# Kernel tuning notes

Hardware: AMD Instinct MI355X
Metric: run time of the kernel (lower is better)

## Reference

```python
import jax, jax.numpy as jnp
import numpy as np

# DRAW-SN dims (enc_size must equal dec_size: mu/sigma Linears declared on dec_size are applied to h_enc)
T, A, B, N = 16, 128, 128, 32
Z, DEC, ENC = 512, 2048, 2048
BATCH = 512
IN_ENC = 2 * N * N + DEC
LOG2PI = float(np.log(2.0 * np.pi))


def setup_inputs() -> dict:
    key = jax.random.key(0)
    k = jax.random.split(key, 14)
    s = 0.02
    return {
        "x": jax.random.uniform(k[0], (BATCH, A * B), dtype=jnp.float32),
        "eps": jax.random.normal(k[1], (T, BATCH, Z), dtype=jnp.float32),
        # PyTorch LSTMCell weights, gate order (i,f,g,o); b = b_ih + b_hh merged
        "enc_Wih": jax.random.normal(k[2], (4 * ENC, IN_ENC), dtype=jnp.float32) * s,
        "enc_Whh": jax.random.normal(k[3], (4 * ENC, ENC), dtype=jnp.float32) * s,
        "enc_b": jax.random.normal(k[4], (4 * ENC,), dtype=jnp.float32) * s,
        "dec_Wih": jax.random.normal(k[5], (4 * DEC, Z), dtype=jnp.float32) * s,
        "dec_Whh": jax.random.normal(k[6], (4 * DEC, DEC), dtype=jnp.float32) * s,
        "dec_b": jax.random.normal(k[7], (4 * DEC,), dtype=jnp.float32) * s,
        "mu_W": jax.random.normal(k[8], (Z, ENC), dtype=jnp.float32) * s,
        "mu_b": jnp.zeros((Z,), jnp.float32),
        "sig_W": jax.random.normal(k[9], (Z, ENC), dtype=jnp.float32) * s,
        "sig_b": jnp.zeros((Z,), jnp.float32),
        "attn_W": jax.random.normal(k[10], (5, DEC), dtype=jnp.float32) * s,
        "attn_b": jnp.zeros((5,), jnp.float32),
        "w_W": jax.random.normal(k[11], (N * N, DEC), dtype=jnp.float32) * s,
        "w_b": jnp.zeros((N * N,), jnp.float32),
    }


def _lstm(xin, h, c, Wih, Whh, b):
    g = xin @ Wih.T + h @ Whh.T + b
    i, f, gg, o = jnp.split(g, 4, axis=1)
    c_new = jax.nn.sigmoid(f) * c + jax.nn.sigmoid(i) * jnp.tanh(gg)
    h_new = jax.nn.sigmoid(o) * jnp.tanh(c_new)
    return h_new, c_new


def _attn(h_dec, attn_W, attn_b):
    p = h_dec @ attn_W.T + attn_b  # (batch, 5)
    gx = (A + 1) / 2 * (p[:, 0] + 1)
    gy = (B + 1) / 2 * (p[:, 1] + 1)
    sigma2 = jnp.exp(p[:, 2])
    delta = (max(A, B) - 1) / (N - 1) * jnp.exp(p[:, 3])
    gamma = jnp.exp(p[:, 4])
    rng = jnp.arange(N, dtype=p.dtype) - N / 2 - 0.5
    mu_x = gx[:, None] + rng * delta[:, None]  # (batch, N)
    mu_y = gy[:, None] + rng * delta[:, None]

    def fmat(size, mu):
        grid = jnp.arange(size, dtype=p.dtype)
        t = (grid[None, None, :] - mu[:, :, None]) / (2 * sigma2[:, None, None])
        F = jnp.exp(-t * t)  # (batch, N, size)
        return F / (jnp.sum(F, axis=2, keepdims=True) + 1e-9)

    return fmat(A, mu_x), fmat(B, mu_y), gamma


def _glimpse(img, Fx, Fy, bsz):
    # Fy (b,N,B) @ img (b,B,A) @ Fx^T (b,A,N) -> (b,N,N)
    return jnp.einsum('bnB,bBa,bma->bnm', Fy, img.reshape(bsz, B, A), Fx).reshape(bsz, N * N)


def _mdl(h):
    # getHistoryStats (history=None -> stats of h itself, COMP=0) + getMDL with RN=True, s=ones
    mean = jnp.mean(h)
    std = jnp.std(h, ddof=1)
    log_p = -0.5 * ((h - mean) / std) ** 2 - jnp.log(std) - 0.5 * LOG2PI
    lse = jax.nn.logsumexp(log_p)
    # both branches of the COMP update equal log(exp(COMP) + sum exp(log_p)) with COMP=0
    COMP = jnp.logaddexp(jnp.float32(0.0), lse)
    l = COMP - lse  # log(s)=0 for s=ones
    return l * h


def reference(x, eps, enc_Wih, enc_Whh, enc_b, dec_Wih, dec_Whh, dec_b,
              mu_W, mu_b, sig_W, sig_b, attn_W, attn_b, w_W, w_b):
    bsz = x.shape[0]

    def step(carry, e):
        h_enc, c_enc, h_dec, c_dec, canvas = carry
        x_hat = x - jax.nn.sigmoid(canvas)
        # read
        Fx, Fy, gamma = _attn(h_dec, attn_W, attn_b)
        r = jnp.concatenate([_glimpse(x, Fx, Fy, bsz) * gamma[:, None],
                             _glimpse(x_hat, Fx, Fy, bsz) * gamma[:, None]], axis=1)
        # encoder + MDL renorm
        h_enc, c_enc = _lstm(jnp.concatenate([r, h_dec], axis=1), h_enc, c_enc,
                             enc_Wih, enc_Whh, enc_b)
        h_enc = _mdl(h_enc)
        # sampleQ
        mu = h_enc @ mu_W.T + mu_b
        sigma = jnp.exp(h_enc @ sig_W.T + sig_b)
        z = mu + sigma * e
        # decoder + MDL renorm
        h_dec_new, c_dec = _lstm(z, h_dec, c_dec, dec_Wih, dec_Whh, dec_b)
        h_dec_new = _mdl(h_dec_new)
        # write: Fy^T @ w @ Fx -> (b,B,A), divided by gamma
        Fx2, Fy2, gamma2 = _attn(h_dec_new, attn_W, attn_b)
        w = (h_dec_new @ w_W.T + w_b).reshape(bsz, N, N)
        wr = jnp.einsum('bnB,bnm,bma->bBa', Fy2, w, Fx2).reshape(bsz, A * B)
        canvas = canvas + wr / gamma2[:, None]
        return (h_enc, c_enc, h_dec_new, c_dec, canvas), None

    init = (jnp.zeros((bsz, ENC), x.dtype), jnp.zeros((bsz, ENC), x.dtype),
            jnp.zeros((bsz, DEC), x.dtype), jnp.zeros((bsz, DEC), x.dtype),
            jnp.zeros((bsz, A * B), x.dtype))
    carry, _ = jax.lax.scan(step, init, eps)
    return carry[4]  # final canvas cs[T-1], shape (batch, A*B)
```

## Files before the change

kernel.cpp:

```cpp
#include <hip/hip_runtime.h>
#include <math.h>

#define BSZ   512
#define TSTEPS 16
#define HID   2048
#define G4    8192
#define ZD    512
#define ABF   16384
#define LOG2PI_F 1.8378770664093453f

typedef float  f32x4  __attribute__((ext_vector_type(4)));
typedef __bf16 bf16x8 __attribute__((ext_vector_type(8)));
typedef unsigned short u16;
typedef u16 u16x4 __attribute__((ext_vector_type(4)));
typedef u16 u16x8v __attribute__((ext_vector_type(8)));
union bfcast { u16x8v u; bf16x8 b; };

__device__ __forceinline__ u16 f2bf(float f){
  union { float f; unsigned u; } v; v.f = f;
  unsigned u = v.u;
  return (u16)((u + 0x7FFFu + ((u >> 16) & 1u)) >> 16);
}
__device__ __forceinline__ float bf2f(u16 u){
  union { unsigned u; float f; } v; v.u = ((unsigned)u) << 16; return v.f;
}
__device__ __forceinline__ float sigm(float x){ return 1.f/(1.f + expf(-x)); }

__device__ __forceinline__ void load_lds16(const void* g, void* l){
  __builtin_amdgcn_global_load_lds(
      (const __attribute__((address_space(1))) void*)g,
      (__attribute__((address_space(3))) void*)l, 16, 0, 0);
}

__device__ __forceinline__ float wsum(float v){
  #pragma unroll
  for (int o = 32; o; o >>= 1) v += __shfl_down(v, o, 64);
  return v;
}

__global__ __launch_bounds__(256) void zero_kernel(float* __restrict__ p, int n4){
  int i = blockIdx.x*256 + threadIdx.x;
  const int st = gridDim.x*256;
  f32x4 z = {0.f,0.f,0.f,0.f};
  for (; i < n4; i += st) ((f32x4*)p)[i] = z;
}

__global__ __launch_bounds__(256) void cvt_kernel(const float* __restrict__ s, u16* __restrict__ d, int n4){
  int i = blockIdx.x*256 + threadIdx.x;
  const int st = gridDim.x*256;
  for (; i < n4; i += st){
    f32x4 v = ((const f32x4*)s)[i];
    u16x4 o;
    o[0]=f2bf(v[0]); o[1]=f2bf(v[1]); o[2]=f2bf(v[2]); o[3]=f2bf(v[3]);
    ((u16x4*)d)[i] = o;
  }
}

__global__ __launch_bounds__(256) void read_fused(
    const u16* __restrict__ x_bf, const float* __restrict__ canvas,
    const u16* __restrict__ h_dec_bf, const float* __restrict__ attnW,
    const float* __restrict__ attn_b, u16* __restrict__ r_bf)
{
  const int b = blockIdx.x;
  const int tid = threadIdx.x;
  const int wave = tid >> 6;
  const int lane = tid & 63;
  const int lr = lane & 15;
  const int lq = lane >> 4;
  __shared__ float red[4][5];
  __shared__ float prm[5];
  __shared__ float rowsum[32][9];
  __shared__ __align__(16) u16 Fxb[32*128];
  __shared__ __align__(16) u16 Fyb[32*128];
  __shared__ __align__(16) u16 Ttx[32*136];
  __shared__ __align__(16) u16 Ttxh[32*136];

  {
    float a0=0,a1=0,a2=0,a3=0,a4=0;
    const u16* h = h_dec_bf + (size_t)b*HID;
    for (int k = tid; k < HID; k += 256){
      const float hv = bf2f(h[k]);
      a0 += hv*attnW[k];
      a1 += hv*attnW[HID + k];
      a2 += hv*attnW[2*HID + k];
      a3 += hv*attnW[3*HID + k];
      a4 += hv*attnW[4*HID + k];
    }
    a0 = wsum(a0); a1 = wsum(a1); a2 = wsum(a2); a3 = wsum(a3); a4 = wsum(a4);
    if (lane == 0){
      red[wave][0]=a0; red[wave][1]=a1; red[wave][2]=a2; red[wave][3]=a3; red[wave][4]=a4;
    }
  }
  __syncthreads();
  if (tid < 5){
    const float p = red[0][tid]+red[1][tid]+red[2][tid]+red[3][tid] + attn_b[tid];
    float v;
    if (tid <= 1)      v = 64.5f*(p + 1.f);
    else if (tid == 2) v = 1.f/(2.f*expf(p));
    else if (tid == 3) v = (127.f/31.f)*expf(p);
    else               v = expf(p);
    prm[tid] = v;
  }
  __syncthreads();
  const float gx = prm[0], gy = prm[1], i2s = prm[2], dl = prm[3], gm = prm[4];

  auto genF = [&](float g0, u16* dst){
    const int rr = tid >> 3;
    const int asub = tid & 7;
    const float mu = g0 + ((float)rr - 16.5f)*dl;
    float s = 0.f;
    for (int a = asub*16; a < asub*16 + 16; a++){
      const float t = ((float)a - mu)*i2s;
      s += expf(-t*t);
    }
    rowsum[rr][asub] = s;
    __syncthreads();
    if (tid < 32){
      float tot = 0.f;
      #pragma unroll
      for (int j = 0; j < 8; j++) tot += rowsum[tid][j];
      rowsum[tid][8] = 1.f/(tot + 1e-9f);
    }
    __syncthreads();
    for (int i = tid; i < 4096; i += 256){
      const int n = i >> 7, a = i & 127;
      const float mu2 = g0 + ((float)n - 16.5f)*dl;
      const float t = ((float)a - mu2)*i2s;
      const float v = expf(-t*t)*rowsum[n][8];
      const int pos = (a >> 3) ^ (n & 7);
      dst[n*128 + pos*8 + (a & 7)] = f2bf(v);
    }
    __syncthreads();
  };
  genF(gx, Fxb);
  genF(gy, Fyb);

  const u16*   xb = x_bf   + (size_t)b*ABF;
  const float* cb = canvas + (size_t)b*ABF;
  f32x4 Cx[2][2], Ch[2][2];
  #pragma unroll
  for (int i = 0; i < 2; i++)
    #pragma unroll
    for (int j = 0; j < 2; j++){ Cx[i][j] = (f32x4){0,0,0,0}; Ch[i][j] = (f32x4){0,0,0,0}; }

  #pragma unroll
  for (int mt = 0; mt < 2; mt++){
    const int row = wave*32 + mt*16 + lr;
    bfcast ax[4], ah[4];
    #pragma unroll
    for (int ks = 0; ks < 4; ks++){
      const int base = row*128 + ks*32 + lq*8;
      ax[ks].u = *(const u16x8v*)&xb[base];
      f32x4 c0 = *(const f32x4*)&cb[base];
      f32x4 c1 = *(const f32x4*)&cb[base + 4];
      #pragma unroll
      for (int j = 0; j < 4; j++){
        ah[ks].u[j]   = f2bf(bf2f(ax[ks].u[j])   - sigm(c0[j]));
        ah[ks].u[4+j] = f2bf(bf2f(ax[ks].u[4+j]) - sigm(c1[j]));
      }
    }
    #pragma unroll
    for (int nt = 0; nt < 2; nt++){
      #pragma unroll
      for (int ks = 0; ks < 4; ks++){
        const int pos = (ks*4 + lq) ^ (lr & 7);
        bf16x8 bf_ = *(const bf16x8*)&Fxb[(nt*16 + lr)*128 + pos*8];
        Cx[mt][nt] = __builtin_amdgcn_mfma_f32_16x16x32_bf16(ax[ks].b, bf_, Cx[mt][nt], 0, 0, 0);
        Ch[mt][nt] = __builtin_amdgcn_mfma_f32_16x16x32_bf16(ah[ks].b, bf_, Ch[mt][nt], 0, 0, 0);
      }
    }
  }
  #pragma unroll
  for (int mt = 0; mt < 2; mt++)
    #pragma unroll
    for (int nt = 0; nt < 2; nt++)
      #pragma unroll
      for (int r = 0; r < 4; r++){
        const int m  = nt*16 + lr;
        const int B_ = wave*32 + mt*16 + lq*4 + r;
        Ttx[m*136 + B_]  = f2bf(Cx[mt][nt][r]);
        Ttxh[m*136 + B_] = f2bf(Ch[mt][nt][r]);
      }
  __syncthreads();

  const int mat = wave >> 1;
  const u16* Tt = mat ? Ttxh : Ttx;
  const int ntl = wave & 1;
  f32x4 R[2];
  R[0] = (f32x4){0,0,0,0}; R[1] = (f32x4){0,0,0,0};
  #pragma unroll
  for (int ks = 0; ks < 4; ks++){
    const int pos = (ks*4 + lq) ^ (lr & 7);
    bf16x8 af = *(const bf16x8*)&Fyb[(ntl*16 + lr)*128 + pos*8];
    #pragma unroll
    for (int mt = 0; mt < 2; mt++){
      bf16x8 bf_ = *(const bf16x8*)&Tt[(mt*16 + lr)*136 + ks*32 + lq*8];
      R[mt] = __builtin_amdgcn_mfma_f32_16x16x32_bf16(af, bf_, R[mt], 0, 0, 0);
    }
  }
  #pragma unroll
  for (int mt = 0; mt < 2; mt++){
    const int m = mt*16 + lr;
    #pragma unroll
    for (int r = 0; r < 4; r++){
      const int n = ntl*16 + lq*4 + r;
      r_bf[(size_t)b*2048 + mat*1024 + n*32 + m] = f2bf(R[mt][r]*gm);
    }
  }
}

struct Slice { const u16* A; const u16* W; const u16* Whi; float* C; int lda, ldw, K, pad; };
struct Slices { Slice s[4]; };

template<int BM, int BN>
__global__ __launch_bounds__(256) void gemm_bt(Slices sl, int nsplit, int ldc)
{
  constexpr int BK = 64;
  constexpr int FI = BM/32;
  constexpr int FJ = BN/32;
  __shared__ __align__(16) u16 Asm[BM*BK];
  __shared__ __align__(16) u16 Bsm[BN*BK];
  const int tid  = threadIdx.x;
  const int wave = tid >> 6;
  const int lane = tid & 63;
  const int wm = wave & 1, wn = wave >> 1;
  const int m0 = blockIdx.y * BM;
  const int n0 = blockIdx.x * BN;
  const Slice& sp = sl.s[blockIdx.z];
  const u16* Ap = sp.A;
  const u16* Wp = sp.W;
  const int lda = sp.lda, ldw = sp.ldw, K = sp.K;
  if (nsplit > 0 && n0 >= nsplit) Wp = sp.Whi - (size_t)nsplit * ldw;
  float* C = sp.C;

  f32x4 acc[FI][FJ];
  #pragma unroll
  for (int i = 0; i < FI; i++)
    #pragma unroll
    for (int j = 0; j < FJ; j++) acc[i][j] = (f32x4){0.f,0.f,0.f,0.f};

  const int lr = lane & 15;
  const int lq = lane >> 4;

  for (int kt = 0; kt < K; kt += BK){
    __syncthreads();
    constexpr int NCA = BM*BK/8;
    #pragma unroll
    for (int it = 0; it < NCA/256; it++){
      const int cb = it*256 + wave*64;
      const int c  = cb + lane;
      const int row = c >> 3;
      const int c8  = (c & 7) ^ (row & 7);
      load_lds16(Ap + (size_t)(m0 + row)*lda + kt + c8*8, &Asm[cb*8]);
    }
    constexpr int NCB = BN*BK/8;
    #pragma unroll
    for (int it = 0; it < NCB/256; it++){
      const int cb = it*256 + wave*64;
      const int c  = cb + lane;
      const int row = c >> 3;
      const int c8  = (c & 7) ^ (row & 7);
      load_lds16(Wp + (size_t)(n0 + row)*ldw + kt + c8*8, &Bsm[cb*8]);
    }
    __syncthreads();
    #pragma unroll
    for (int ks = 0; ks < 2; ks++){
      bf16x8 af[FI], bfr[FJ];
      #pragma unroll
      for (int i = 0; i < FI; i++){
        const int row = wm*(BM/2) + i*16 + lr;
        const int xx = (ks*4 + lq) ^ (row & 7);
        af[i] = *(const bf16x8*)&Asm[row*BK + xx*8];
      }
      #pragma unroll
      for (int j = 0; j < FJ; j++){
        const int row = wn*(BN/2) + j*16 + lr;
        const int xx = (ks*4 + lq) ^ (row & 7);
        bfr[j] = *(const bf16x8*)&Bsm[row*BK + xx*8];
      }
      #pragma unroll
      for (int i = 0; i < FI; i++)
        #pragma unroll
        for (int j = 0; j < FJ; j++)
          acc[i][j] = __builtin_amdgcn_mfma_f32_16x16x32_bf16(af[i], bfr[j], acc[i][j], 0, 0, 0);
    }
  }
  #pragma unroll
  for (int i = 0; i < FI; i++){
    const int gm = m0 + wm*(BM/2) + i*16 + lq*4;
    #pragma unroll
    for (int j = 0; j < FJ; j++){
      const int gn = n0 + wn*(BN/2) + j*16 + lr;
      #pragma unroll
      for (int r = 0; r < 4; r++)
        C[(size_t)(gm + r)*ldc + gn] = acc[i][j][r];
    }
  }
}

__global__ __launch_bounds__(256) void lstm_kernel(
    const float* __restrict__ g, const float* __restrict__ bias,
    float* __restrict__ c, float* __restrict__ h, float* __restrict__ ps)
{
  const int idx = blockIdx.x*256 + threadIdx.x;
  const int m = idx >> 9;
  const int q = idx & 511;
  const size_t gb = (size_t)m*G4 + q*4;
  const float* g1 = g + 4194304;
  const float* g2 = g + 2*4194304;
  f32x4 gi = *(const f32x4*)&g[gb]         + *(const f32x4*)&g1[gb]         + *(const f32x4*)&g2[gb]         + *(const f32x4*)&bias[q*4];
  f32x4 gf = *(const f32x4*)&g[gb+HID]     + *(const f32x4*)&g1[gb+HID]     + *(const f32x4*)&g2[gb+HID]     + *(const f32x4*)&bias[HID+q*4];
  f32x4 gg = *(const f32x4*)&g[gb+2*HID]   + *(const f32x4*)&g1[gb+2*HID]   + *(const f32x4*)&g2[gb+2*HID]   + *(const f32x4*)&bias[2*HID+q*4];
  f32x4 go = *(const f32x4*)&g[gb+3*HID]   + *(const f32x4*)&g1[gb+3*HID]   + *(const f32x4*)&g2[gb+3*HID]   + *(const f32x4*)&bias[3*HID+q*4];
  const size_t cb = (size_t)m*HID + q*4;
  f32x4 cv = *(const f32x4*)&c[cb];
  f32x4 cn, hn;
  #pragma unroll
  for (int k = 0; k < 4; k++){
    const float ck = sigm(gf[k])*cv[k] + sigm(gi[k])*tanhf(gg[k]);
    cn[k] = ck;
    hn[k] = sigm(go[k])*tanhf(ck);
  }
  *(f32x4*)&c[cb] = cn;
  *(f32x4*)&h[cb] = hn;
  float s1 = hn[0]+hn[1]+hn[2]+hn[3];
  float s2 = hn[0]*hn[0]+hn[1]*hn[1]+hn[2]*hn[2]+hn[3]*hn[3];
  s1 = wsum(s1); s2 = wsum(s2);
  __shared__ float r1[4], r2[4];
  const int w = threadIdx.x >> 6;
  if ((threadIdx.x & 63) == 0){ r1[w] = s1; r2[w] = s2; }
  __syncthreads();
  if (threadIdx.x == 0){
    ps[blockIdx.x]        = r1[0]+r1[1]+r1[2]+r1[3];
    ps[1024 + blockIdx.x] = r2[0]+r2[1]+r2[2]+r2[3];
  }
}

__global__ __launch_bounds__(256) void sumexp_kernel(
    const float* __restrict__ h, const float* __restrict__ ps, float* __restrict__ pe)
{
  const int tid = threadIdx.x;
  float t1 = 0.f, t2 = 0.f;
  for (int i = tid; i < 1024; i += 256){ t1 += ps[i]; t2 += ps[1024 + i]; }
  t1 = wsum(t1); t2 = wsum(t2);
  __shared__ float r1[4], r2[4];
  const int w = tid >> 6;
  if ((tid & 63) == 0){ r1[w] = t1; r2[w] = t2; }
  __syncthreads();
  __shared__ float mh[2];
  if (tid == 0){
    const float S1 = r1[0]+r1[1]+r1[2]+r1[3];
    const float S2 = r2[0]+r2[1]+r2[2]+r2[3];
    const float mean = S1*(1.f/1048576.f);
    const float var  = (S2 - 1048576.f*mean*mean)*(1.f/1048575.f);
    mh[0] = mean; mh[1] = 1.f/sqrtf(var);
  }
  __syncthreads();
  const float mean = mh[0], istd = mh[1];
  float se = 0.f;
  for (int i = blockIdx.x*256 + tid; i < (1<<18); i += 256*256){
    f32x4 v = ((const f32x4*)h)[i];
    #pragma unroll
    for (int k = 0; k < 4; k++){
      const float u = (v[k] - mean)*istd;
      se += expf(-0.5f*u*u);
    }
  }
  se = wsum(se);
  __shared__ float r3[4];
  if ((tid & 63) == 0) r3[w] = se;
  __syncthreads();
  if (tid == 0) pe[blockIdx.x] = r3[0]+r3[1]+r3[2]+r3[3];
}

__global__ __launch_bounds__(256) void scale_kernel(
    const float* __restrict__ h, const float* __restrict__ ps,
    const float* __restrict__ pe, u16* __restrict__ hb)
{
  const int tid = threadIdx.x;
  float t1 = 0.f, t2 = 0.f;
  for (int i = tid; i < 1024; i += 256){ t1 += ps[i]; t2 += ps[1024 + i]; }
  float t3 = pe[tid];
  t1 = wsum(t1); t2 = wsum(t2); t3 = wsum(t3);
  __shared__ float r1[4], r2[4], r3[4];
  const int w = tid >> 6;
  if ((tid & 63) == 0){ r1[w] = t1; r2[w] = t2; r3[w] = t3; }
  __syncthreads();
  __shared__ float lsh;
  if (tid == 0){
    const float S1 = r1[0]+r1[1]+r1[2]+r1[3];
    const float S2 = r2[0]+r2[1]+r2[2]+r2[3];
    const float SE = r3[0]+r3[1]+r3[2]+r3[3];
    const float mean = S1*(1.f/1048576.f);
    const float var  = (S2 - 1048576.f*mean*mean)*(1.f/1048575.f);
    const float stdv = sqrtf(var);
    const float lse = logf(SE) - logf(stdv) - 0.5f*LOG2PI_F;
    lsh = fmaxf(-lse, 0.f) + log1pf(expf(-fabsf(lse)));
  }
  __syncthreads();
  const float l = lsh;
  const int i = blockIdx.x*256 + tid;
  f32x4 v = ((const f32x4*)h)[i];
  u16x4 o;
  #pragma unroll
  for (int k = 0; k < 4; k++) o[k] = f2bf(v[k]*l);
  ((u16x4*)hb)[i] = o;
}

__global__ __launch_bounds__(256) void z_kernel(
    const float* __restrict__ zp, const float* __restrict__ mu_b,
    const float* __restrict__ sig_b, const float* __restrict__ ep, u16* __restrict__ zo)
{
  const int idx = blockIdx.x*256 + threadIdx.x;
  const int m = idx >> 7;
  const int q = idx & 127;
  const size_t base = (size_t)m*1024 + q*4;
  f32x4 mu = *(const f32x4*)&zp[base] + *(const f32x4*)&zp[524288 + base]
           + *(const f32x4*)&zp[2*524288 + base] + *(const f32x4*)&zp[3*524288 + base]
           + *(const f32x4*)&mu_b[q*4];
  f32x4 ls = *(const f32x4*)&zp[base+512] + *(const f32x4*)&zp[524288 + base+512]
           + *(const f32x4*)&zp[2*524288 + base+512] + *(const f32x4*)&zp[3*524288 + base+512]
           + *(const f32x4*)&sig_b[q*4];
  f32x4 ev = *(const f32x4*)&ep[(size_t)m*512 + q*4];
  u16x4 o;
  #pragma unroll
  for (int k = 0; k < 4; k++) o[k] = f2bf(mu[k] + expf(ls[k])*ev[k]);
  ((u16x4*)zo)[idx] = o;
}

__global__ __launch_bounds__(256) void write_fused(
    const float* __restrict__ wp, const float* __restrict__ w_b,
    const u16* __restrict__ h_dec_bf, const float* __restrict__ attnW,
    const float* __restrict__ attn_b, float* __restrict__ canvas)
{
  const int b = blockIdx.x;
  const int tid = threadIdx.x;
  __shared__ float red[4][5];
  __shared__ float prm[5];
  __shared__ float inv[32];
  __shared__ float sW[1024];
  __shared__ __align__(16) float sF[32*132];
  __shared__ float sU[128*33];

  {
    float a0=0,a1=0,a2=0,a3=0,a4=0;
    const u16* h = h_dec_bf + (size_t)b*HID;
    for (int k = tid; k < HID; k += 256){
      const float hv = bf2f(h[k]);
      a0 += hv*attnW[k];
      a1 += hv*attnW[HID + k];
      a2 += hv*attnW[2*HID + k];
      a3 += hv*attnW[3*HID + k];
      a4 += hv*attnW[4*HID + k];
    }
    a0 = wsum(a0); a1 = wsum(a1); a2 = wsum(a2); a3 = wsum(a3); a4 = wsum(a4);
    if ((tid & 63) == 0){
      const int w = tid >> 6;
      red[w][0]=a0; red[w][1]=a1; red[w][2]=a2; red[w][3]=a3; red[w][4]=a4;
    }
  }
  for (int i = tid; i < 1024; i += 256)
    sW[i] = wp[(size_t)b*1024 + i] + wp[524288 + (size_t)b*1024 + i]
          + wp[2*524288 + (size_t)b*1024 + i] + wp[3*524288 + (size_t)b*1024 + i] + w_b[i];
  __syncthreads();
  if (tid < 5){
    const float p = red[0][tid]+red[1][tid]+red[2][tid]+red[3][tid] + attn_b[tid];
    float v;
    if (tid <= 1)      v = 64.5f*(p + 1.f);
    else if (tid == 2) v = 1.f/(2.f*expf(p));
    else if (tid == 3) v = (127.f/31.f)*expf(p);
    else               v = expf(p);
    prm[tid] = v;
  }
  __syncthreads();
  const float gx = prm[0], gy = prm[1], i2s = prm[2], dl = prm[3], gm = prm[4];

  auto genF = [&](float g0){
    for (int i = tid; i < 4096; i += 256){
      const int n = i >> 7, a = i & 127;
      const float mu = g0 + ((float)n - 16.5f)*dl;
      const float t = ((float)a - mu)*i2s;
      sF[n*132 + a] = expf(-t*t);
    }
    __syncthreads();
    if (tid < 32){
      float ssum = 0.f;
      for (int a = 0; a < 128; a++) ssum += sF[tid*132 + a];
      inv[tid] = 1.f/(ssum + 1e-9f);
    }
    __syncthreads();
    for (int i = tid; i < 4096; i += 256)
      sF[(i >> 7)*132 + (i & 127)] *= inv[i >> 7];
    __syncthreads();
  };

  genF(gy);
  {
    const int Bg = tid & 31, mg = tid >> 5;
    float acc[4][4] = {};
    for (int n = 0; n < 32; n++){
      float fy[4], wv[4];
      #pragma unroll
      for (int i = 0; i < 4; i++) fy[i] = sF[n*132 + Bg + 32*i];
      #pragma unroll
      for (int j = 0; j < 4; j++) wv[j] = sW[n*32 + mg*4 + j];
      #pragma unroll
      for (int i = 0; i < 4; i++)
        #pragma unroll
        for (int j = 0; j < 4; j++) acc[i][j] += fy[i]*wv[j];
    }
    #pragma unroll
    for (int i = 0; i < 4; i++)
      #pragma unroll
      for (int j = 0; j < 4; j++)
        sU[(Bg + 32*i)*33 + mg*4 + j] = acc[i][j];
  }
  __syncthreads();
  genF(gx);
  {
    const int Bg = tid & 31, ag = tid >> 5;
    float acc[64];
    #pragma unroll
    for (int k = 0; k < 64; k++) acc[k] = 0.f;
    for (int mm = 0; mm < 32; mm++){
      float u[4];
      #pragma unroll
      for (int i = 0; i < 4; i++) u[i] = sU[(Bg + 32*i)*33 + mm];
      f32x4 fx[4];
      #pragma unroll
      for (int k = 0; k < 4; k++) fx[k] = *(const f32x4*)&sF[mm*132 + ag*16 + k*4];
      #pragma unroll
      for (int i = 0; i < 4; i++)
        #pragma unroll
        for (int k = 0; k < 4; k++)
          #pragma unroll
          for (int cc = 0; cc < 4; cc++)
            acc[i*16 + k*4 + cc] += u[i]*fx[k][cc];
    }
    const float ig = 1.f/gm;
    #pragma unroll
    for (int i = 0; i < 4; i++){
      const int B_ = Bg + 32*i;
      #pragma unroll
      for (int k = 0; k < 4; k++){
        float* cp = &canvas[(size_t)b*ABF + B_*128 + ag*16 + k*4];
        f32x4 cv = *(const f32x4*)cp;
        #pragma unroll
        for (int cc = 0; cc < 4; cc++) cv[cc] += acc[i*16 + k*4 + cc]*ig;
        *(f32x4*)cp = cv;
      }
    }
  }
}

extern "C" void kernel_launch(void* const* d_in, const int* in_sizes, int n_in,
                              void* d_out, int out_size, void* d_ws, size_t ws_size,
                              hipStream_t stream)
{
  (void)in_sizes; (void)n_in; (void)out_size; (void)ws_size;
  const float* x      = (const float*)d_in[0];
  const float* eps    = (const float*)d_in[1];
  const float* encWih = (const float*)d_in[2];
  const float* encWhh = (const float*)d_in[3];
  const float* enc_b  = (const float*)d_in[4];
  const float* decWih = (const float*)d_in[5];
  const float* decWhh = (const float*)d_in[6];
  const float* dec_b  = (const float*)d_in[7];
  const float* muW    = (const float*)d_in[8];
  const float* mu_b   = (const float*)d_in[9];
  const float* sigW   = (const float*)d_in[10];
  const float* sig_b  = (const float*)d_in[11];
  const float* attnW  = (const float*)d_in[12];
  const float* attn_b = (const float*)d_in[13];
  const float* wW     = (const float*)d_in[14];
  const float* w_b    = (const float*)d_in[15];
  float* canvas = (float*)d_out;

  char* wsb = (char*)d_ws;
  size_t off = 0;
  auto alloc = [&](size_t bytes)->char*{
    char* p = wsb + off; off += (bytes + 255) & ~(size_t)255; return p;
  };
  float* c_enc    = (float*)alloc(1048576*4);
  float* c_dec    = (float*)alloc(1048576*4);
  u16*   h_enc_bf = (u16*)  alloc(1048576*2);
  u16*   h_dec_bf = (u16*)  alloc(1048576*2);
  const size_t state_bytes = off;
  float* ps    = (float*)alloc(2304*4);
  float* pe    = (float*)alloc(256*4);
  float* h_tmp = (float*)alloc(1048576*4);
  float* g_buf = (float*)alloc((size_t)3*4194304*4);
  u16*   r_bf  = (u16*)  alloc(1048576*2);
  u16*   z_bf  = (u16*)  alloc(262144*2);
  float* zbuf  = (float*)alloc((size_t)4*524288*4);
  float* wbuf  = (float*)alloc((size_t)4*524288*4);
  u16*   x_bf  = (u16*)  alloc((size_t)8388608*2);
  u16* wih_bf  = (u16*)alloc((size_t)33554432*2);
  u16* whh_bf  = (u16*)alloc((size_t)16777216*2);
  u16* dwih_bf = (u16*)alloc((size_t)4194304*2);
  u16* dwhh_bf = (u16*)alloc((size_t)16777216*2);
  u16* muw_bf  = (u16*)alloc((size_t)1048576*2);
  u16* sigw_bf = (u16*)alloc((size_t)1048576*2);
  u16* ww_bf   = (u16*)alloc((size_t)2097152*2);

  zero_kernel<<<1024, 256, 0, stream>>>((float*)wsb, (int)(state_bytes/16));
  zero_kernel<<<2048, 256, 0, stream>>>(canvas, (ABF/4)*BSZ);
  cvt_kernel<<<2048, 256, 0, stream>>>(x,      x_bf,    8388608/4);
  cvt_kernel<<<2048, 256, 0, stream>>>(encWih, wih_bf,  33554432/4);
  cvt_kernel<<<2048, 256, 0, stream>>>(encWhh, whh_bf,  16777216/4);
  cvt_kernel<<<1024, 256, 0, stream>>>(decWih, dwih_bf, 4194304/4);
  cvt_kernel<<<2048, 256, 0, stream>>>(decWhh, dwhh_bf, 16777216/4);
  cvt_kernel<<<512,  256, 0, stream>>>(muW,    muw_bf,  1048576/4);
  cvt_kernel<<<512,  256, 0, stream>>>(sigW,   sigw_bf, 1048576/4);
  cvt_kernel<<<512,  256, 0, stream>>>(wW,     ww_bf,   2097152/4);

  float* g0 = g_buf;
  float* g1 = g_buf + 4194304;
  float* g2 = g_buf + 2*4194304;

  Slices enc_sl = {};
  enc_sl.s[0] = { r_bf,            wih_bf,          nullptr, g0, HID, 2*HID, HID, 0 };
  enc_sl.s[1] = { h_dec_bf,        wih_bf + HID,    nullptr, g1, HID, 2*HID, HID, 0 };
  enc_sl.s[2] = { h_enc_bf,        whh_bf,          nullptr, g2, HID, HID,   HID, 0 };

  Slices dec_sl = {};
  dec_sl.s[0] = { z_bf,            dwih_bf,         nullptr, g0, ZD,  ZD,    ZD,   0 };
  dec_sl.s[1] = { h_dec_bf,        dwhh_bf,         nullptr, g1, HID, HID,   1024, 0 };
  dec_sl.s[2] = { h_dec_bf + 1024, dwhh_bf + 1024,  nullptr, g2, HID, HID,   1024, 0 };

  Slices ms_sl = {}, w_sl = {};
  for (int k = 0; k < 4; k++){
    ms_sl.s[k] = { h_enc_bf + 512*k, muw_bf + 512*k, sigw_bf + 512*k, zbuf + (size_t)k*524288, HID, HID, 512, 0 };
    w_sl.s[k]  = { h_dec_bf + 512*k, ww_bf  + 512*k, nullptr,         wbuf + (size_t)k*524288, HID, HID, 512, 0 };
  }

  for (int t = 0; t < TSTEPS; t++){
    read_fused<<<512, 256, 0, stream>>>(x_bf, canvas, h_dec_bf, attnW, attn_b, r_bf);
    gemm_bt<64,128><<<dim3(64,8,3), 256, 0, stream>>>(enc_sl, 0, G4);
    lstm_kernel<<<1024, 256, 0, stream>>>(g_buf, enc_b, c_enc, h_tmp, ps);
    sumexp_kernel<<<256, 256, 0, stream>>>(h_tmp, ps, pe);
    scale_kernel<<<1024, 256, 0, stream>>>(h_tmp, ps, pe, h_enc_bf);
    gemm_bt<64,64><<<dim3(16,8,4), 256, 0, stream>>>(ms_sl, 512, 1024);
    z_kernel<<<256, 256, 0, stream>>>(zbuf, mu_b, sig_b, eps + (size_t)t*BSZ*ZD, z_bf);
    gemm_bt<64,128><<<dim3(64,8,3), 256, 0, stream>>>(dec_sl, 0, G4);
    lstm_kernel<<<1024, 256, 0, stream>>>(g_buf, dec_b, c_dec, h_tmp, ps);
    sumexp_kernel<<<256, 256, 0, stream>>>(h_tmp, ps, pe);
    scale_kernel<<<1024, 256, 0, stream>>>(h_tmp, ps, pe, h_dec_bf);
    gemm_bt<64,64><<<dim3(16,8,4), 256, 0, stream>>>(w_sl, 0, 1024);
    write_fused<<<512, 256, 0, stream>>>(wbuf, w_b, h_dec_bf, attnW, attn_b, canvas);
  }
}
```

Measured before the change: 4.342 ms.

## Concatenate LSTM inputs and weights, use 256x256 double-buffered split-K GEMM

Packs the encoder input [r, h_dec, h_enc] and decoder input [z, h_dec] into single concatenated activation buffers, with matching concatenated bf16 weight matrices. The LSTM gate GEMMs then run as one uniform 4-way split-K problem on a new 256x256-tile, 512-thread, LDS double-buffered MFMA kernel. The LSTM kernel sums four partial buffers instead of three. This aims to raise arithmetic intensity and balance work across slices. The cost is an extra partial-sum read and write, plus a scale kernel that writes h_dec to two places.

After: 4.137 ms. -4.7%, faster.

```diff
diff --git a/kernel.cpp b/kernel.cpp
--- a/kernel.cpp
+++ b/kernel.cpp
@@ -7,6 +7,8 @@
 #define G4    8192
 #define ZD    512
 #define ABF   16384
+#define ENCK  6144
+#define DECK  2560
 #define LOG2PI_F 1.8378770664093453f
 
 typedef float  f32x4  __attribute__((ext_vector_type(4)));
@@ -56,10 +58,26 @@
   }
 }
 
+__global__ __launch_bounds__(256) void cvt_strided_kernel(
+    const float* __restrict__ s, u16* __restrict__ d,
+    int n4, int sh, int cmask, int dstride, int coloff)
+{
+  int i = blockIdx.x*256 + threadIdx.x;
+  const int st = gridDim.x*256;
+  for (; i < n4; i += st){
+    f32x4 v = ((const f32x4*)s)[i];
+    u16x4 o;
+    o[0]=f2bf(v[0]); o[1]=f2bf(v[1]); o[2]=f2bf(v[2]); o[3]=f2bf(v[3]);
+    const int row = i >> sh;
+    const int c4  = i & cmask;
+    *(u16x4*)&d[(size_t)row*dstride + coloff + c4*4] = o;
+  }
+}
+
 __global__ __launch_bounds__(256) void read_fused(
     const u16* __restrict__ x_bf, const float* __restrict__ canvas,
-    const u16* __restrict__ h_dec_bf, const float* __restrict__ attnW,
-    const float* __restrict__ attn_b, u16* __restrict__ r_bf)
+    const u16* __restrict__ hd, const float* __restrict__ attnW,
+    const float* __restrict__ attn_b, u16* __restrict__ r_out)
 {
   const int b = blockIdx.x;
   const int tid = threadIdx.x;
@@ -77,7 +95,7 @@
 
   {
     float a0=0,a1=0,a2=0,a3=0,a4=0;
-    const u16* h = h_dec_bf + (size_t)b*HID;
+    const u16* h = hd + (size_t)b*DECK;
     for (int k = tid; k < HID; k += 256){
       const float hv = bf2f(h[k]);
       a0 += hv*attnW[k];
@@ -204,7 +222,7 @@
     #pragma unroll
     for (int r = 0; r < 4; r++){
       const int n = ntl*16 + lq*4 + r;
-      r_bf[(size_t)b*2048 + mat*1024 + n*32 + m] = f2bf(R[mt][r]*gm);
+      r_out[(size_t)b*ENCK + mat*1024 + n*32 + m] = f2bf(R[mt][r]*gm);
     }
   }
 }
@@ -298,6 +316,109 @@
   }
 }
 
+__global__ __launch_bounds__(512, 2) void gemm256(Slices sl, int ldc)
+{
+  __shared__ __align__(16) u16 Asm[2][256*64];
+  __shared__ __align__(16) u16 Bsm[2][256*64];
+  const int tid  = threadIdx.x;
+  const int wave = tid >> 6;
+  const int lane = tid & 63;
+  const int lr = lane & 15;
+  const int lq = lane >> 4;
+  const int wm = wave >> 2;
+  const int wn = wave & 3;
+
+  const int bid = blockIdx.x;
+  const int wg  = (bid & 7)*32 + (bid >> 3);
+  const int bx  = wg & 31;
+  const int by  = (wg >> 5) & 1;
+  const int bz  = wg >> 6;
+  const int m0 = by*256, n0 = bx*256;
+  const Slice& sp = sl.s[bz];
+  const u16* __restrict__ Ap = sp.A;
+  const u16* __restrict__ Wp = sp.W;
+  float* __restrict__ C = sp.C;
+  const int lda = sp.lda, ldw = sp.ldw;
+  const int nt = sp.K >> 6;
+
+  f32x4 acc[8][4];
+  #pragma unroll
+  for (int i = 0; i < 8; i++)
+    #pragma unroll
+    for (int j = 0; j < 4; j++) acc[i][j] = (f32x4){0.f,0.f,0.f,0.f};
+
+  auto stage = [&](int kt, int bsel){
+    const int kcol = kt << 6;
+    #pragma unroll
+    for (int it = 0; it < 4; it++){
+      const int cbk = it*512 + wave*64;
+      const int c   = cbk + lane;
+      const int row = c >> 3;
+      const int c8  = (c & 7) ^ (row & 7);
+      load_lds16(Ap + (size_t)(m0 + row)*lda + kcol + c8*8, &Asm[bsel][cbk*8]);
+    }
+    #pragma unroll
+    for (int it = 0; it < 4; it++){
+      const int cbk = it*512 + wave*64;
+      const int c   = cbk + lane;
+      const int row = c >> 3;
+      const int c8  = (c & 7) ^ (row & 7);
+      load_lds16(Wp + (size_t)(n0 + row)*ldw + kcol + c8*8, &Bsm[bsel][cbk*8]);
+    }
+  };
+
+  stage(0, 0);
+  for (int t = 0; t < nt; t++){
+    const int cur = t & 1;
+    if (t + 1 < nt){
+      stage(t + 1, cur ^ 1);
+      __builtin_amdgcn_sched_barrier(0);
+      asm volatile("s_waitcnt vmcnt(8)" ::: "memory");
+    } else {
+      asm volatile("s_waitcnt vmcnt(0)" ::: "memory");
+    }
+    __builtin_amdgcn_s_barrier();
+    __builtin_amdgcn_sched_barrier(0);
+
+    bf16x8 bfr[2][4];
+    #pragma unroll
+    for (int ks = 0; ks < 2; ks++)
+      #pragma unroll
+      for (int j = 0; j < 4; j++){
+        const int row = wn*64 + j*16 + lr;
+        const int xx = (ks*4 + lq) ^ (row & 7);
+        bfr[ks][j] = *(const bf16x8*)&Bsm[cur][row*64 + xx*8];
+      }
+    #pragma unroll
+    for (int i = 0; i < 8; i++){
+      const int row = wm*128 + i*16 + lr;
+      const bf16x8 a0 = *(const bf16x8*)&Asm[cur][row*64 + ((lq    ) ^ (row & 7))*8];
+      const bf16x8 a1 = *(const bf16x8*)&Asm[cur][row*64 + ((4 + lq) ^ (row & 7))*8];
+      __builtin_amdgcn_s_setprio(1);
+      #pragma unroll
+      for (int j = 0; j < 4; j++){
+        acc[i][j] = __builtin_amdgcn_mfma_f32_16x16x32_bf16(a0, bfr[0][j], acc[i][j], 0, 0, 0);
+        acc[i][j] = __builtin_amdgcn_mfma_f32_16x16x32_bf16(a1, bfr[1][j], acc[i][j], 0, 0, 0);
+      }
+      __builtin_amdgcn_s_setprio(0);
+    }
+    __builtin_amdgcn_sched_barrier(0);
+    __builtin_amdgcn_s_barrier();
+  }
+
+  #pragma unroll
+  for (int i = 0; i < 8; i++){
+    const int gmr = m0 + wm*128 + i*16 + lq*4;
+    #pragma unroll
+    for (int j = 0; j < 4; j++){
+      const int gn = n0 + wn*64 + j*16 + lr;
+      #pragma unroll
+      for (int r = 0; r < 4; r++)
+        C[(size_t)(gmr + r)*ldc + gn] = acc[i][j][r];
+    }
+  }
+}
+
 __global__ __launch_bounds__(256) void lstm_kernel(
     const float* __restrict__ g, const float* __restrict__ bias,
     float* __restrict__ c, float* __restrict__ h, float* __restrict__ ps)
@@ -308,10 +429,11 @@
   const size_t gb = (size_t)m*G4 + q*4;
   const float* g1 = g + 4194304;
   const float* g2 = g + 2*4194304;
-  f32x4 gi = *(const f32x4*)&g[gb]         + *(const f32x4*)&g1[gb]         + *(const f32x4*)&g2[gb]         + *(const f32x4*)&bias[q*4];
-  f32x4 gf = *(const f32x4*)&g[gb+HID]     + *(const f32x4*)&g1[gb+HID]     + *(const f32x4*)&g2[gb+HID]     + *(const f32x4*)&bias[HID+q*4];
-  f32x4 gg = *(const f32x4*)&g[gb+2*HID]   + *(const f32x4*)&g1[gb+2*HID]   + *(const f32x4*)&g2[gb+2*HID]   + *(const f32x4*)&bias[2*HID+q*4];
-  f32x4 go = *(const f32x4*)&g[gb+3*HID]   + *(const f32x4*)&g1[gb+3*HID]   + *(const f32x4*)&g2[gb+3*HID]   + *(const f32x4*)&bias[3*HID+q*4];
+  const float* g3 = g + 3*4194304;
+  f32x4 gi = *(const f32x4*)&g[gb]         + *(const f32x4*)&g1[gb]         + *(const f32x4*)&g2[gb]         + *(const f32x4*)&g3[gb]         + *(const f32x4*)&bias[q*4];
+  f32x4 gf = *(const f32x4*)&g[gb+HID]     + *(const f32x4*)&g1[gb+HID]     + *(const f32x4*)&g2[gb+HID]     + *(const f32x4*)&g3[gb+HID]     + *(const f32x4*)&bias[HID+q*4];
+  f32x4 gg = *(const f32x4*)&g[gb+2*HID]   + *(const f32x4*)&g1[gb+2*HID]   + *(const f32x4*)&g2[gb+2*HID]   + *(const f32x4*)&g3[gb+2*HID]   + *(const f32x4*)&bias[2*HID+q*4];
+  f32x4 go = *(const f32x4*)&g[gb+3*HID]   + *(const f32x4*)&g1[gb+3*HID]   + *(const f32x4*)&g2[gb+3*HID]   + *(const f32x4*)&g3[gb+3*HID]   + *(const f32x4*)&bias[3*HID+q*4];
   const size_t cb = (size_t)m*HID + q*4;
   f32x4 cv = *(const f32x4*)&c[cb];
   f32x4 cn, hn;
@@ -375,7 +497,8 @@
 
 __global__ __launch_bounds__(256) void scale_kernel(
     const float* __restrict__ h, const float* __restrict__ ps,
-    const float* __restrict__ pe, u16* __restrict__ hb)
+    const float* __restrict__ pe, u16* __restrict__ d1, int ld1,
+    u16* __restrict__ d2, int ld2)
 {
   const int tid = threadIdx.x;
   float t1 = 0.f, t2 = 0.f;
@@ -400,11 +523,14 @@
   __syncthreads();
   const float l = lsh;
   const int i = blockIdx.x*256 + tid;
+  const int row = i >> 9;
+  const int c4  = i & 511;
   f32x4 v = ((const f32x4*)h)[i];
   u16x4 o;
   #pragma unroll
   for (int k = 0; k < 4; k++) o[k] = f2bf(v[k]*l);
-  ((u16x4*)hb)[i] = o;
+  *(u16x4*)&d1[(size_t)row*ld1 + c4*4] = o;
+  if (d2) *(u16x4*)&d2[(size_t)row*ld2 + c4*4] = o;
 }
 
 __global__ __launch_bounds__(256) void z_kernel(
@@ -425,12 +551,12 @@
   u16x4 o;
   #pragma unroll
   for (int k = 0; k < 4; k++) o[k] = f2bf(mu[k] + expf(ls[k])*ev[k]);
-  ((u16x4*)zo)[idx] = o;
+  *(u16x4*)&zo[(size_t)m*DECK + q*4] = o;
 }
 
 __global__ __launch_bounds__(256) void write_fused(
     const float* __restrict__ wp, const float* __restrict__ w_b,
-    const u16* __restrict__ h_dec_bf, const float* __restrict__ attnW,
+    const u16* __restrict__ hd, const float* __restrict__ attnW,
     const float* __restrict__ attn_b, float* __restrict__ canvas)
 {
   const int b = blockIdx.x;
@@ -444,7 +570,7 @@
 
   {
     float a0=0,a1=0,a2=0,a3=0,a4=0;
-    const u16* h = h_dec_bf + (size_t)b*HID;
+    const u16* h = hd + (size_t)b*DECK;
     for (int k = tid; k < HID; k += 256){
       const float hv = bf2f(h[k]);
       a0 += hv*attnW[k];
@@ -581,72 +707,62 @@
   auto alloc = [&](size_t bytes)->char*{
     char* p = wsb + off; off += (bytes + 255) & ~(size_t)255; return p;
   };
-  float* c_enc    = (float*)alloc(1048576*4);
-  float* c_dec    = (float*)alloc(1048576*4);
-  u16*   h_enc_bf = (u16*)  alloc(1048576*2);
-  u16*   h_dec_bf = (u16*)  alloc(1048576*2);
+  float* c_enc = (float*)alloc(1048576*4);
+  float* c_dec = (float*)alloc(1048576*4);
+  u16*   encA  = (u16*)  alloc((size_t)BSZ*ENCK*2);
+  u16*   decA  = (u16*)  alloc((size_t)BSZ*DECK*2);
   const size_t state_bytes = off;
   float* ps    = (float*)alloc(2304*4);
   float* pe    = (float*)alloc(256*4);
   float* h_tmp = (float*)alloc(1048576*4);
-  float* g_buf = (float*)alloc((size_t)3*4194304*4);
-  u16*   r_bf  = (u16*)  alloc(1048576*2);
-  u16*   z_bf  = (u16*)  alloc(262144*2);
-  float* zbuf  = (float*)alloc((size_t)4*524288*4);
-  float* wbuf  = (float*)alloc((size_t)4*524288*4);
+  float* g_buf = (float*)alloc((size_t)4*4194304*4);
+  float* zbuf  = g_buf;
+  float* wbuf  = g_buf + 2097152;
   u16*   x_bf  = (u16*)  alloc((size_t)8388608*2);
-  u16* wih_bf  = (u16*)alloc((size_t)33554432*2);
-  u16* whh_bf  = (u16*)alloc((size_t)16777216*2);
-  u16* dwih_bf = (u16*)alloc((size_t)4194304*2);
-  u16* dwhh_bf = (u16*)alloc((size_t)16777216*2);
+  u16* encW    = (u16*)alloc((size_t)G4*ENCK*2);
+  u16* decW    = (u16*)alloc((size_t)G4*DECK*2);
   u16* muw_bf  = (u16*)alloc((size_t)1048576*2);
   u16* sigw_bf = (u16*)alloc((size_t)1048576*2);
   u16* ww_bf   = (u16*)alloc((size_t)2097152*2);
 
   zero_kernel<<<1024, 256, 0, stream>>>((float*)wsb, (int)(state_bytes/16));
   zero_kernel<<<2048, 256, 0, stream>>>(canvas, (ABF/4)*BSZ);
-  cvt_kernel<<<2048, 256, 0, stream>>>(x,      x_bf,    8388608/4);
-  cvt_kernel<<<2048, 256, 0, stream>>>(encWih, wih_bf,  33554432/4);
-  cvt_kernel<<<2048, 256, 0, stream>>>(encWhh, whh_bf,  16777216/4);
-  cvt_kernel<<<1024, 256, 0, stream>>>(decWih, dwih_bf, 4194304/4);
-  cvt_kernel<<<2048, 256, 0, stream>>>(decWhh, dwhh_bf, 16777216/4);
-  cvt_kernel<<<512,  256, 0, stream>>>(muW,    muw_bf,  1048576/4);
-  cvt_kernel<<<512,  256, 0, stream>>>(sigW,   sigw_bf, 1048576/4);
-  cvt_kernel<<<512,  256, 0, stream>>>(wW,     ww_bf,   2097152/4);
-
-  float* g0 = g_buf;
-  float* g1 = g_buf + 4194304;
-  float* g2 = g_buf + 2*4194304;
+  cvt_kernel<<<2048, 256, 0, stream>>>(x,    x_bf,   8388608/4);
+  cvt_strided_kernel<<<2048, 256, 0, stream>>>(encWih, encW, 8388608, 10, 1023, ENCK, 0);
+  cvt_strided_kernel<<<2048, 256, 0, stream>>>(encWhh, encW, 4194304,  9,  511, ENCK, 4096);
+  cvt_strided_kernel<<<1024, 256, 0, stream>>>(decWih, decW, 1048576,  7,  127, DECK, 0);
+  cvt_strided_kernel<<<2048, 256, 0, stream>>>(decWhh, decW, 4194304,  9,  511, DECK, 512);
+  cvt_kernel<<<512,  256, 0, stream>>>(muW,  muw_bf,  1048576/4);
+  cvt_kernel<<<512,  256, 0, stream>>>(sigW, sigw_bf, 1048576/4);
+  cvt_kernel<<<512,  256, 0, stream>>>(wW,   ww_bf,   2097152/4);
 
   Slices enc_sl = {};
-  enc_sl.s[0] = { r_bf,            wih_bf,          nullptr, g0, HID, 2*HID, HID, 0 };
-  enc_sl.s[1] = { h_dec_bf,        wih_bf + HID,    nullptr, g1, HID, 2*HID, HID, 0 };
-  enc_sl.s[2] = { h_enc_bf,        whh_bf,          nullptr, g2, HID, HID,   HID, 0 };
+  for (int k = 0; k < 4; k++)
+    enc_sl.s[k] = { encA + 1536*k, encW + 1536*k, nullptr, g_buf + (size_t)k*4194304, ENCK, ENCK, 1536, 0 };
 
   Slices dec_sl = {};
-  dec_sl.s[0] = { z_bf,            dwih_bf,         nullptr, g0, ZD,  ZD,    ZD,   0 };
-  dec_sl.s[1] = { h_dec_bf,        dwhh_bf,         nullptr, g1, HID, HID,   1024, 0 };
-  dec_sl.s[2] = { h_dec_bf + 1024, dwhh_bf + 1024,  nullptr, g2, HID, HID,   1024, 0 };
+  for (int k = 0; k < 4; k++)
+    dec_sl.s[k] = { decA + 640*k, decW + 640*k, nullptr, g_buf + (size_t)k*4194304, DECK, DECK, 640, 0 };
 
   Slices ms_sl = {}, w_sl = {};
   for (int k = 0; k < 4; k++){
-    ms_sl.s[k] = { h_enc_bf + 512*k, muw_bf + 512*k, sigw_bf + 512*k, zbuf + (size_t)k*524288, HID, HID, 512, 0 };
-    w_sl.s[k]  = { h_dec_bf + 512*k, ww_bf  + 512*k, nullptr,         wbuf + (size_t)k*524288, HID, HID, 512, 0 };
+    ms_sl.s[k] = { encA + 4096 + 512*k, muw_bf + 512*k, sigw_bf + 512*k, zbuf + (size_t)k*524288, ENCK, HID, 512, 0 };
+    w_sl.s[k]  = { decA + 512  + 512*k, ww_bf  + 512*k, nullptr,         wbuf + (size_t)k*524288, DECK, HID, 512, 0 };
   }
 
   for (int t = 0; t < TSTEPS; t++){
-    read_fused<<<512, 256, 0, stream>>>(x_bf, canvas, h_dec_bf, attnW, attn_b, r_bf);
-    gemm_bt<64,128><<<dim3(64,8,3), 256, 0, stream>>>(enc_sl, 0, G4);
+    read_fused<<<512, 256, 0, stream>>>(x_bf, canvas, decA + 512, attnW, attn_b, encA);
+    gemm256<<<256, 512, 0, stream>>>(enc_sl, G4);
     lstm_kernel<<<1024, 256, 0, stream>>>(g_buf, enc_b, c_enc, h_tmp, ps);
     sumexp_kernel<<<256, 256, 0, stream>>>(h_tmp, ps, pe);
-    scale_kernel<<<1024, 256, 0, stream>>>(h_tmp, ps, pe, h_enc_bf);
+    scale_kernel<<<1024, 256, 0, stream>>>(h_tmp, ps, pe, encA + 4096, ENCK, nullptr, 0);
     gemm_bt<64,64><<<dim3(16,8,4), 256, 0, stream>>>(ms_sl, 512, 1024);
-    z_kernel<<<256, 256, 0, stream>>>(zbuf, mu_b, sig_b, eps + (size_t)t*BSZ*ZD, z_bf);
-    gemm_bt<64,128><<<dim3(64,8,3), 256, 0, stream>>>(dec_sl, 0, G4);
+    z_kernel<<<256, 256, 0, stream>>>(zbuf, mu_b, sig_b, eps + (size_t)t*BSZ*ZD, decA);
+    gemm256<<<256, 512, 0, stream>>>(dec_sl, G4);
     lstm_kernel<<<1024, 256, 0, stream>>>(g_buf, dec_b, c_dec, h_tmp, ps);
     sumexp_kernel<<<256, 256, 0, stream>>>(h_tmp, ps, pe);
-    scale_kernel<<<1024, 256, 0, stream>>>(h_tmp, ps, pe, h_dec_bf);
+    scale_kernel<<<1024, 256, 0, stream>>>(h_tmp, ps, pe, decA + 512, DECK, encA + 2048, ENCK);
     gemm_bt<64,64><<<dim3(16,8,4), 256, 0, stream>>>(w_sl, 0, 1024);
-    write_fused<<<512, 256, 0, stream>>>(wbuf, w_b, h_dec_bf, attnW, attn_b, canvas);
-  }
-}
+    write_fused<<<512, 256, 0, stream>>>(wbuf, w_b, decA + 512, attnW, attn_b, canvas);
+  }
+}
```
